# Optimization experiments

Hardware: AMD Instinct MI355X
Metric: run time of the kernel (lower is better)

## Reference

```python
import jax, jax.numpy as jnp
import numpy as np

D = 1024  # feature_size

def setup_inputs() -> dict:
    key = jax.random.key(0)
    ks = jax.random.split(key, 9)
    s = 1.0 / np.sqrt(D)
    inp = {"x": jax.random.normal(ks[0], (4, 2048, D), dtype=jnp.float32)}
    names = ["Wk", "Wq", "Wv", "Wo"]
    for i, n in enumerate(names):
        inp[n] = jax.random.uniform(ks[1 + 2 * i], (D, D), dtype=jnp.float32, minval=-s, maxval=s)
        inp["b" + n[1]] = jax.random.uniform(ks[2 + 2 * i], (D,), dtype=jnp.float32, minval=-s, maxval=s)
    return inp

def reference(x, Wk, bk, Wq, bq, Wv, bv, Wo, bo):
    # Linear layers: x @ W.T + b (torch nn.Linear convention)
    keys = jnp.einsum('bsd,ed->bse', x, Wk) + bk
    queries = jnp.einsum('bsd,ed->bse', x, Wq) + bq
    values = jnp.einsum('bsd,ed->bse', x, Wv) + bv
    scale = 1.0 / jnp.sqrt(jnp.float32(D))
    scores = jnp.einsum('bqd,bkd->bqk', queries, keys) * scale  # [B,S,S]
    attention = jax.nn.softmax(scores, axis=-1)
    out = jnp.einsum('bqk,bkd->bqd', attention, values)
    out = jnp.einsum('bsd,ed->bse', out, Wo) + bo
    return (out, attention)
```

## Files before the change

kernel.cpp:

```cpp
#include <hip/hip_runtime.h>
#include <hip/hip_bf16.h>


typedef __attribute__((ext_vector_type(8))) _Float16 f16x8;
typedef __attribute__((ext_vector_type(4))) _Float16 f16x4;
typedef __attribute__((ext_vector_type(4))) float f32x4;

static __device__ __forceinline__ void gl_lds16(const void* g, void* s) {
  __builtin_amdgcn_global_load_lds(
      (const __attribute__((address_space(1))) void*)g,
      (__attribute__((address_space(3))) void*)s, 16, 0, 0);
}

__global__ __launch_bounds__(256) void prep(
    const float* __restrict__ x,
    const float* __restrict__ Wq, const float* __restrict__ Wk,
    const float* __restrict__ Wo, const float* __restrict__ Wv,
    const float* __restrict__ bv, const float* __restrict__ bo,
    _Float16* __restrict__ xh, _Float16* __restrict__ Woh,
    _Float16* __restrict__ WvT, _Float16* __restrict__ WqT,
    _Float16* __restrict__ WkT, float* __restrict__ cpb) {
  const int b = blockIdx.x;
  const int tid = threadIdx.x;
  if (b < 8192) {
    const int i = b * 256 + tid;
    float4 v = reinterpret_cast<const float4*>(x)[i];
    f16x4 r = {(_Float16)v.x, (_Float16)v.y, (_Float16)v.z, (_Float16)v.w};
    reinterpret_cast<f16x4*>(xh)[i] = r;
  } else if (b < 9216) {
    const int i = (b - 8192) * 256 + tid;
    float4 v = reinterpret_cast<const float4*>(Wo)[i];
    f16x4 r = {(_Float16)v.x, (_Float16)v.y, (_Float16)v.z, (_Float16)v.w};
    reinterpret_cast<f16x4*>(Woh)[i] = r;
  } else if (b < 9984) {
    const int bb = b - 9216;
    const int which = bb >> 8;
    const float* src = which == 0 ? Wv : which == 1 ? Wq : Wk;
    _Float16* dst = which == 0 ? WvT : which == 1 ? WqT : WkT;
    __shared__ float t[64][65];
    const int tb = bb & 255;
    const int bx = (tb & 15) * 64, by = (tb >> 4) * 64;
    const int tx = tid & 63, ty = tid >> 6;
#pragma unroll
    for (int i = 0; i < 64; i += 4)
      t[ty + i][tx] = src[(long)(by + ty + i) * 1024 + bx + tx];
    __syncthreads();
#pragma unroll
    for (int i = 0; i < 64; i += 4)
      dst[(long)(bx + ty + i) * 1024 + by + tx] = (_Float16)t[tx][ty + i];
  } else {
    const int n = b - 9984;
    float s = 0.f;
    for (int d = tid; d < 1024; d += 256) s += Wo[(long)n * 1024 + d] * bv[d];
#pragma unroll
    for (int o = 32; o >= 1; o >>= 1) s += __shfl_xor(s, o);
    __shared__ float red[4];
    if ((tid & 63) == 0) red[tid >> 6] = s;
    __syncthreads();
    if (tid == 0) cpb[n] = red[0] + red[1] + red[2] + red[3] + bo[n];
  }
}

__global__ __launch_bounds__(256) void wkern(
    const float* __restrict__ bq, const float* __restrict__ bk,
    const _Float16* __restrict__ WkT, const _Float16* __restrict__ WqT,
    float* __restrict__ w1, float* __restrict__ w2, float* __restrict__ c0) {
  const int b = blockIdx.x;
  const int tid = threadIdx.x;
  float s = 0.f;
  if (b < 1024) {
    for (int e = tid; e < 1024; e += 256) s += bq[e] * (float)WkT[(long)b * 1024 + e];
  } else if (b < 2048) {
    const int d = b - 1024;
    for (int e = tid; e < 1024; e += 256) s += bk[e] * (float)WqT[(long)d * 1024 + e];
  } else {
    for (int e = tid; e < 1024; e += 256) s += bq[e] * bk[e];
  }
#pragma unroll
  for (int o = 32; o >= 1; o >>= 1) s += __shfl_xor(s, o);
  __shared__ float red[4];
  if ((tid & 63) == 0) red[tid >> 6] = s;
  __syncthreads();
  if (tid == 0) {
    const float v = red[0] + red[1] + red[2] + red[3];
    if (b < 1024) w1[b] = v;
    else if (b < 2048) w2[b - 1024] = v;
    else c0[0] = v;
  }
}

__global__ __launch_bounds__(256) void rowcol(
    const _Float16* __restrict__ xh, const float* __restrict__ w1,
    const float* __restrict__ w2, const float* __restrict__ c0,
    float* __restrict__ rowb, float* __restrict__ colb) {
  const long i = blockIdx.x;
  const int tid = threadIdx.x;
  f16x4 xv = reinterpret_cast<const f16x4*>(xh + i * 1024)[tid];
  float4 a1 = reinterpret_cast<const float4*>(w1)[tid];
  float4 a2 = reinterpret_cast<const float4*>(w2)[tid];
  float x0 = (float)xv[0], x1 = (float)xv[1], x2 = (float)xv[2], x3 = (float)xv[3];
  float d1 = x0 * a1.x + x1 * a1.y + x2 * a1.z + x3 * a1.w;
  float d2 = x0 * a2.x + x1 * a2.y + x2 * a2.z + x3 * a2.w;
#pragma unroll
  for (int o = 32; o >= 1; o >>= 1) { d1 += __shfl_xor(d1, o); d2 += __shfl_xor(d2, o); }
  __shared__ float r1[4], r2[4];
  if ((tid & 63) == 0) { r1[tid >> 6] = d1; r2[tid >> 6] = d2; }
  __syncthreads();
  if (tid == 0) {
    colb[i] = (r1[0] + r1[1] + r1[2] + r1[3]) * 0.03125f;
    rowb[i] = (r2[0] + r2[1] + r2[2] + r2[3] + c0[0]) * 0.03125f;
  }
}

template <int EPI>
__global__ __launch_bounds__(512, 2) void gemm256p8(
    const _Float16* __restrict__ A, const _Float16* __restrict__ B,
    const float* __restrict__ colb, const float* __restrict__ rowb,
    _Float16* __restrict__ Ch, _Float16* __restrict__ C3,
    int M, int N, int K, long sA, long sB, long sC, float alpha) {
  __shared__ _Float16 lds[2][2][2][8192];

  const unsigned gx = gridDim.x, gy = gridDim.y;
  const unsigned nwg = gx * gy * gridDim.z;
  unsigned flat = (blockIdx.z * gy + blockIdx.y) * gx + blockIdx.x;
  flat = (flat & 7) * (nwg >> 3) + (flat >> 3);
  const long bz = flat / (gx * gy);
  const unsigned rem = flat % (gx * gy);
  const unsigned byi = rem % gy;
  const unsigned bxi = rem / gy;

  const int tid = threadIdx.x;
  const int w = tid >> 6, lane = tid & 63;
  const int wr = w >> 2, wc = w & 3;
  const int lr = lane & 15, q = lane >> 4;
  const long row0 = (long)byi * 256;
  const long col0 = (long)bxi * 256;
  const int nt = K >> 6;

  const _Float16* pA = A + bz * sA;
  const _Float16* pB = B + bz * sB;

  f32x4 acc[8][4] = {};

  const int r0 = tid >> 2, c0i = ((tid & 3) - (r0 >> 1)) & 3;
  const int s1 = tid + 512;
  const int r1 = s1 >> 2, c1 = ((s1 & 3) - (r1 >> 1)) & 3;

  auto stage = [&](int t, int ab, int kk) {
    if (t >= nt) return;
    const int d = t & 1;
    const _Float16* src = ab ? pB : pA;
    const long base = ab ? col0 : row0;
    const long gk = (long)t * 64 + kk * 32;
    gl_lds16(src + (base + r0) * (long)K + gk + c0i * 8, &lds[d][ab][kk][w << 9]);
    gl_lds16(src + (base + r1) * (long)K + gk + c1 * 8,
             &lds[d][ab][kk][4096 + (w << 9)]);
  };
  auto rd = [&](int d, int ab, int kk, int r) -> f16x8 {
    const int slot = (r << 2) + ((q + (r >> 1)) & 3);
    return *(const f16x8*)&lds[d][ab][kk][slot << 3];
  };

#define PH_SYNC()                                         \
  __builtin_amdgcn_s_barrier();                           \
  asm volatile("s_waitcnt lgkmcnt(0)" ::: "memory");      \
  __builtin_amdgcn_sched_barrier(0);                      \
  __builtin_amdgcn_s_setprio(1);
#define PH_END()                                          \
  __builtin_amdgcn_s_setprio(0);                          \
  __builtin_amdgcn_sched_barrier(0);                      \
  __builtin_amdgcn_s_barrier();

  stage(0, 0, 0); stage(0, 1, 0); stage(0, 0, 1); stage(0, 1, 1);
  stage(1, 1, 0); stage(1, 0, 0); stage(1, 1, 1);
  asm volatile("s_waitcnt vmcnt(6)" ::: "memory");
  __builtin_amdgcn_s_barrier();
  __builtin_amdgcn_sched_barrier(0);

  f16x8 a[4], b[4];
  for (int t = 0; t < nt; ++t) {
    const int d = t & 1;
#pragma unroll
    for (int mi = 0; mi < 4; ++mi) a[mi] = rd(d, 0, 0, wr * 128 + mi * 16 + lr);
#pragma unroll
    for (int n = 0; n < 4; ++n) b[n] = rd(d, 1, 0, wc * 64 + n * 16 + lr);
    stage(t + 1, 0, 1);
    PH_SYNC();
#pragma unroll
    for (int mi = 0; mi < 4; ++mi)
#pragma unroll
      for (int n = 0; n < 4; ++n)
        acc[mi][n] = __builtin_amdgcn_mfma_f32_16x16x32_f16(a[mi], b[n], acc[mi][n], 0, 0, 0);
    PH_END();
#pragma unroll
    for (int mi = 0; mi < 4; ++mi) a[mi] = rd(d, 0, 0, wr * 128 + 64 + mi * 16 + lr);
    stage(t + 2, 1, 0);
    PH_SYNC();
#pragma unroll
    for (int mi = 0; mi < 4; ++mi)
#pragma unroll
      for (int n = 0; n < 4; ++n)
        acc[4 + mi][n] = __builtin_amdgcn_mfma_f32_16x16x32_f16(a[mi], b[n], acc[4 + mi][n], 0, 0, 0);
    PH_END();
#pragma unroll
    for (int mi = 0; mi < 4; ++mi) a[mi] = rd(d, 0, 1, wr * 128 + mi * 16 + lr);
#pragma unroll
    for (int n = 0; n < 4; ++n) b[n] = rd(d, 1, 1, wc * 64 + n * 16 + lr);
    stage(t + 2, 0, 0);
    PH_SYNC();
#pragma unroll
    for (int mi = 0; mi < 4; ++mi)
#pragma unroll
      for (int n = 0; n < 4; ++n)
        acc[mi][n] = __builtin_amdgcn_mfma_f32_16x16x32_f16(a[mi], b[n], acc[mi][n], 0, 0, 0);
    PH_END();
#pragma unroll
    for (int mi = 0; mi < 4; ++mi) a[mi] = rd(d, 0, 1, wr * 128 + 64 + mi * 16 + lr);
    stage(t + 2, 1, 1);
    PH_SYNC();
#pragma unroll
    for (int mi = 0; mi < 4; ++mi)
#pragma unroll
      for (int n = 0; n < 4; ++n)
        acc[4 + mi][n] = __builtin_amdgcn_mfma_f32_16x16x32_f16(a[mi], b[n], acc[4 + mi][n], 0, 0, 0);
    __builtin_amdgcn_s_setprio(0);
    __builtin_amdgcn_sched_barrier(0);
    if (t + 2 < nt) asm volatile("s_waitcnt vmcnt(6)" ::: "memory");
    else            asm volatile("s_waitcnt vmcnt(0)" ::: "memory");
    __builtin_amdgcn_s_barrier();
    __builtin_amdgcn_sched_barrier(0);
  }
#undef PH_SYNC
#undef PH_END

  if (EPI == 2) {
#pragma unroll
    for (int mi = 0; mi < 8; ++mi)
#pragma unroll
      for (int n = 0; n < 4; ++n)
#pragma unroll
        for (int r = 0; r < 4; ++r) {
          const long row = row0 + wr * 128 + mi * 16 + q * 4 + r;
          const long col = col0 + wc * 64 + n * 16 + lr;
          float v = acc[mi][n][r] * alpha;
          v += rowb[bz * 2048 + row] + colb[bz * 2048 + col];
          Ch[bz * sC + row * (long)N + col] = (_Float16)v;
        }
  } else {
    if (col0 < 1024) {
#pragma unroll
      for (int mi = 0; mi < 8; ++mi)
#pragma unroll
        for (int n = 0; n < 4; ++n)
#pragma unroll
          for (int r = 0; r < 4; ++r) {
            const long row = row0 + wr * 128 + mi * 16 + q * 4 + r;
            const long col = col0 + wc * 64 + n * 16 + lr;
            Ch[row * 1024 + col] = (_Float16)(acc[mi][n][r] * alpha);
          }
    } else {
      _Float16* wb = ((_Float16*)lds) + w * 4224;
      const long b2 = row0 >> 11;
      const long s2b = (row0 & 2047) + wr * 128;
#pragma unroll
      for (int ch = 0; ch < 2; ++ch) {
#pragma unroll
        for (int nn = 0; nn < 2; ++nn) {
          const int n = ch * 2 + nn;
#pragma unroll
          for (int mi = 0; mi < 8; ++mi)
#pragma unroll
            for (int r = 0; r < 4; ++r) {
              const int cl = nn * 16 + lr;
              const int rl = mi * 16 + q * 4 + r;
              wb[cl * 132 + rl] = (_Float16)(acc[mi][n][r] * alpha);
            }
        }
        asm volatile("s_waitcnt lgkmcnt(0)" ::: "memory");
        __builtin_amdgcn_sched_barrier(0);
        const int cl = lane >> 1, sseg = (lane & 1) * 64;
        _Float16* dst = C3 +
            (b2 * 1024 + (col0 - 1024) + wc * 64 + ch * 32 + cl) * 2048 + s2b + sseg;
        const _Float16* srcp = wb + cl * 132 + sseg;
#pragma unroll
        for (int j = 0; j < 8; ++j)
          *(f16x8*)(dst + j * 8) = *(const f16x8*)(srcp + j * 8);
      }
    }
  }
}

__global__ __launch_bounds__(512, 1) void pv128x256(
    const _Float16* __restrict__ P, const _Float16* __restrict__ V,
    const float* __restrict__ cpb, float* __restrict__ out, int K) {
  __shared__ _Float16 lds[2][2][12288];

  const unsigned gx = gridDim.x, gy = gridDim.y;
  const unsigned nwg = gx * gy;
  unsigned flat = blockIdx.y * gx + blockIdx.x;
  flat = (flat & 7) * (nwg >> 3) + (flat >> 3);
  const unsigned byi = flat % gy;
  const unsigned bxi = flat / gy;

  const int tid = threadIdx.x;
  const int w = tid >> 6, lane = tid & 63;
  const int wr = w >> 2, wc = w & 3;
  const int lr = lane & 15, q = lane >> 4;
  const long row0 = (long)byi * 128;
  const long col0 = (long)bxi * 256;
  const int nt = K >> 6;

  const _Float16* pA = P + row0 * (long)K;
  const _Float16* pB = V + (row0 >> 11) * 2097152L + col0 * (long)K;

  f32x4 acc[4][4] = {};

  const int rA = tid >> 2, cA = ((tid & 3) - (rA >> 1)) & 3;
  const int sB1 = tid + 512;
  const int rB1 = sB1 >> 2, cB1 = ((sB1 & 3) - (rB1 >> 1)) & 3;

  auto stage = [&](int t, int kk) {
    if (t >= nt) return;
    const int d = t & 1;
    const long gk = (long)t * 64 + kk * 32;
    gl_lds16(pA + rA * (long)K + gk + cA * 8, &lds[d][kk][w << 9]);
    gl_lds16(pB + rA * (long)K + gk + cA * 8, &lds[d][kk][4096 + (w << 9)]);
    gl_lds16(pB + rB1 * (long)K + gk + cB1 * 8, &lds[d][kk][8192 + (w << 9)]);
  };
  auto rdA = [&](int d, int kk, int r) -> f16x8 {
    const int slot = (r << 2) + ((q + (r >> 1)) & 3);
    return *(const f16x8*)&lds[d][kk][slot << 3];
  };
  auto rdB = [&](int d, int kk, int r) -> f16x8 {
    const int slot = (r << 2) + ((q + (r >> 1)) & 3);
    return *(const f16x8*)&lds[d][kk][4096 * 8 / 8 + (slot << 3)];
  };

#define PH_SYNC()                                         \
  __builtin_amdgcn_s_barrier();                           \
  asm volatile("s_waitcnt lgkmcnt(0)" ::: "memory");      \
  __builtin_amdgcn_sched_barrier(0);                      \
  __builtin_amdgcn_s_setprio(1);

  stage(0, 0); stage(0, 1); stage(1, 0);
  asm volatile("s_waitcnt vmcnt(6)" ::: "memory");
  __builtin_amdgcn_s_barrier();
  __builtin_amdgcn_sched_barrier(0);

  f16x8 a[4], b[4];
  for (int t = 0; t < nt; ++t) {
    const int d = t & 1;
#pragma unroll
    for (int mi = 0; mi < 4; ++mi) a[mi] = rdA(d, 0, wr * 64 + mi * 16 + lr);
#pragma unroll
    for (int n = 0; n < 4; ++n) b[n] = rdB(d, 0, wc * 64 + n * 16 + lr);
    stage(t + 1, 1);
    PH_SYNC();
#pragma unroll
    for (int mi = 0; mi < 4; ++mi)
#pragma unroll
      for (int n = 0; n < 4; ++n)
        acc[mi][n] = __builtin_amdgcn_mfma_f32_16x16x32_f16(a[mi], b[n], acc[mi][n], 0, 0, 0);
    __builtin_amdgcn_s_setprio(0);
    __builtin_amdgcn_sched_barrier(0);
    if (t + 1 < nt) asm volatile("s_waitcnt vmcnt(6)" ::: "memory");
    else            asm volatile("s_waitcnt vmcnt(0)" ::: "memory");
    __builtin_amdgcn_s_barrier();
    __builtin_amdgcn_sched_barrier(0);
#pragma unroll
    for (int mi = 0; mi < 4; ++mi) a[mi] = rdA(d, 1, wr * 64 + mi * 16 + lr);
#pragma unroll
    for (int n = 0; n < 4; ++n) b[n] = rdB(d, 1, wc * 64 + n * 16 + lr);
    stage(t + 2, 0);
    PH_SYNC();
#pragma unroll
    for (int mi = 0; mi < 4; ++mi)
#pragma unroll
      for (int n = 0; n < 4; ++n)
        acc[mi][n] = __builtin_amdgcn_mfma_f32_16x16x32_f16(a[mi], b[n], acc[mi][n], 0, 0, 0);
    __builtin_amdgcn_s_setprio(0);
    __builtin_amdgcn_sched_barrier(0);
    if (t + 2 < nt)      asm volatile("s_waitcnt vmcnt(6)" ::: "memory");
    else if (t + 1 < nt) asm volatile("s_waitcnt vmcnt(3)" ::: "memory");
    else                 asm volatile("s_waitcnt vmcnt(0)" ::: "memory");
    __builtin_amdgcn_s_barrier();
    __builtin_amdgcn_sched_barrier(0);
  }
#undef PH_SYNC

#pragma unroll
  for (int mi = 0; mi < 4; ++mi)
#pragma unroll
    for (int n = 0; n < 4; ++n)
#pragma unroll
      for (int r = 0; r < 4; ++r) {
        const long row = row0 + wr * 64 + mi * 16 + q * 4 + r;
        const long col = col0 + wc * 64 + n * 16 + lr;
        out[row * 1024 + col] = acc[mi][n][r] + cpb[col];
      }
}

template <int EPI, int BSH>
__global__ __launch_bounds__(256) void gemm128(
    const _Float16* __restrict__ A, const _Float16* __restrict__ B,
    const float* __restrict__ bias, float* __restrict__ Cf,
    _Float16* __restrict__ Ch,
    int M, int N, int K, long sA, long sB, long sC, float alpha, int panelW) {
  __shared__ _Float16 lds[3][2][4096];

  const unsigned gx = gridDim.x, gy = gridDim.y;
  const unsigned nwg = gx * gy * gridDim.z;
  unsigned flat = (blockIdx.z * gy + blockIdx.y) * gx + blockIdx.x;
  flat = (flat & 7) * (nwg >> 3) + (flat >> 3);
  const unsigned pb = gy * panelW;
  const long bz = flat / (gx * gy);
  const unsigned rem = flat % (gx * gy);
  const unsigned pi = rem / pb;
  const unsigned rem2 = rem % pb;
  const unsigned byi = rem2 / panelW;
  const unsigned bxi = pi * panelW + rem2 % panelW;

  const int tid = threadIdx.x;
  const int w = tid >> 6, lane = tid & 63;
  const int wr = w >> 1, wc = w & 1;
  const int lr = lane & 15, q = lane >> 4;
  const long row0 = (long)byi * 128;
  const long col0 = (long)bxi * 128;
  const int nt = K >> 5;

  const _Float16* pA = A + bz * sA;
  const _Float16* pB = BSH ? (B + (row0 >> BSH) * sB) : (B + bz * sB);

  f32x4 acc[4][4] = {};

  const int r0 = tid >> 2, c0i = ((tid & 3) - (r0 >> 1)) & 3;
  const int s1 = tid + 256;
  const int r1 = s1 >> 2, c1 = ((s1 & 3) - (r1 >> 1)) & 3;

  auto stage = [&](int kt) {
    if (kt >= nt) return;
    const int bf = kt % 3;
    const long gk = (long)kt * 32;
#pragma unroll
    for (int ab = 0; ab < 2; ++ab) {
      const _Float16* src = ab ? pB : pA;
      const long base = ab ? col0 : row0;
      gl_lds16(src + (base + r0) * (long)K + gk + c0i * 8, &lds[bf][ab][w << 9]);
      gl_lds16(src + (base + r1) * (long)K + gk + c1 * 8, &lds[bf][ab][2048 + (w << 9)]);
    }
  };
  auto rd = [&](int bf, int ab, int r) -> f16x8 {
    const int slot = (r << 2) + ((q + (r >> 1)) & 3);
    return *(const f16x8*)&lds[bf][ab][slot << 3];
  };

  stage(0); stage(1);
  asm volatile("s_waitcnt vmcnt(4)" ::: "memory");
  __builtin_amdgcn_s_barrier();
  __builtin_amdgcn_sched_barrier(0);

  for (int kt = 0; kt < nt; ++kt) {
    const int bf = kt % 3;
    stage(kt + 2);
    f16x8 a[4], b[4];
#pragma unroll
    for (int m = 0; m < 4; ++m) a[m] = rd(bf, 0, wr * 64 + m * 16 + lr);
#pragma unroll
    for (int n = 0; n < 4; ++n) b[n] = rd(bf, 1, wc * 64 + n * 16 + lr);
#pragma unroll
    for (int m = 0; m < 4; ++m)
#pragma unroll
      for (int n = 0; n < 4; ++n)
        acc[m][n] = __builtin_amdgcn_mfma_f32_16x16x32_f16(a[m], b[n], acc[m][n], 0, 0, 0);
    if (kt < nt - 2) asm volatile("s_waitcnt vmcnt(4)" ::: "memory");
    else             asm volatile("s_waitcnt vmcnt(0)" ::: "memory");
    __builtin_amdgcn_s_barrier();
    __builtin_amdgcn_sched_barrier(0);
  }

#pragma unroll
  for (int m = 0; m < 4; ++m)
#pragma unroll
    for (int n = 0; n < 4; ++n)
#pragma unroll
      for (int r = 0; r < 4; ++r) {
        const long row = row0 + wr * 64 + m * 16 + q * 4 + r;
        const long col = col0 + wc * 64 + n * 16 + lr;
        float v = acc[m][n][r] * alpha;
        if (bias) v += bias[col];
        if (EPI == 0) Cf[bz * sC + row * (long)N + col] = v;
        else          Ch[bz * sC + row * (long)N + col] = (_Float16)v;
      }
}

__global__ __launch_bounds__(256) void softmax16(
    _Float16* __restrict__ Ph, float* __restrict__ attn) {
  const long row = blockIdx.x;
  _Float16* ph = Ph + row * 2048;
  float* ap = attn + row * 2048;
  const int tid = threadIdx.x;
  f16x8 v = reinterpret_cast<const f16x8*>(ph)[tid];
  float x[8];
#pragma unroll
  for (int j = 0; j < 8; ++j) x[j] = (float)v[j];
  float m = x[0];
#pragma unroll
  for (int j = 1; j < 8; ++j) m = fmaxf(m, x[j]);
#pragma unroll
  for (int o = 32; o >= 1; o >>= 1) m = fmaxf(m, __shfl_xor(m, o));
  __shared__ float red[4], red2[4];
  if ((tid & 63) == 0) red[tid >> 6] = m;
  __syncthreads();
  m = fmaxf(fmaxf(red[0], red[1]), fmaxf(red[2], red[3]));
  float s = 0.f;
#pragma unroll
  for (int j = 0; j < 8; ++j) { x[j] = expf(x[j] - m); s += x[j]; }
#pragma unroll
  for (int o = 32; o >= 1; o >>= 1) s += __shfl_xor(s, o);
  if ((tid & 63) == 0) red2[tid >> 6] = s;
  __syncthreads();
  s = red2[0] + red2[1] + red2[2] + red2[3];
  const float inv = 1.0f / s;
#pragma unroll
  for (int j = 0; j < 8; ++j) x[j] *= inv;
  reinterpret_cast<float4*>(ap)[tid * 2] = make_float4(x[0], x[1], x[2], x[3]);
  reinterpret_cast<float4*>(ap)[tid * 2 + 1] = make_float4(x[4], x[5], x[6], x[7]);
  f16x8 pv;
#pragma unroll
  for (int j = 0; j < 8; ++j) pv[j] = (_Float16)x[j];
  reinterpret_cast<f16x8*>(ph)[tid] = pv;
}

extern "C" void kernel_launch(void* const* d_in, const int* in_sizes, int n_in,
                              void* d_out, int out_size, void* d_ws, size_t ws_size,
                              hipStream_t stream) {
  const float* x  = (const float*)d_in[0];
  const float* Wk = (const float*)d_in[1];
  const float* bk = (const float*)d_in[2];
  const float* Wq = (const float*)d_in[3];
  const float* bq = (const float*)d_in[4];
  const float* Wv = (const float*)d_in[5];
  const float* bv = (const float*)d_in[6];
  const float* Wo = (const float*)d_in[7];
  const float* bo = (const float*)d_in[8];

  float* out  = (float*)d_out;
  float* attn = (float*)d_out + 8388608;

  const size_t MB = 1024 * 1024;
  unsigned char* ws = (unsigned char*)d_ws;
  _Float16* xh   = (_Float16*)(ws + 0 * MB);
  _Float16* Wf   = (_Float16*)(ws + 16 * MB);
  _Float16* WkT  = (_Float16*)(ws + 20 * MB);
  _Float16* Woh  = (_Float16*)(ws + 22 * MB);
  _Float16* WqT  = (_Float16*)(ws + 24 * MB);
  _Float16* WvT  = (_Float16*)(ws + 26 * MB);
  float*    rowb = (float*)   (ws + 28 * MB);
  float*    colb = (float*)   (ws + 28 * MB + 32768);
  float*    cpb  = (float*)   (ws + 28 * MB + 65536);
  float*    w1   = (float*)   (ws + 28 * MB + 69632);
  float*    w2   = (float*)   (ws + 28 * MB + 73728);
  float*    c0s  = (float*)   (ws + 28 * MB + 77824);
  _Float16* Y    = (_Float16*)(ws + 29 * MB);
  _Float16* Vt   = (_Float16*)(ws + 45 * MB);
  _Float16* Ph   = (_Float16*)(ws + 61 * MB);

  dim3 blk(256);
  dim3 blk5(512);
  const _Float16* nullh = nullptr;

  hipLaunchKernelGGL(prep, dim3(11008), blk, 0, stream,
                     x, Wq, Wk, Wo, Wv, bv, bo, xh, Woh, WvT, WqT, WkT, cpb);
  hipLaunchKernelGGL(wkern, dim3(2049), blk, 0, stream, bq, bk, WkT, WqT, w1, w2, c0s);
  hipLaunchKernelGGL((gemm128<1, 10>), dim3(8, 16, 1), blk, 0, stream,
                     WkT, WqT, (const float*)nullptr, (float*)nullptr, Wf,
                     2048, 1024, 1024, 0L, 1048576L, 0L, 1.0f, 8);
  hipLaunchKernelGGL(rowcol, dim3(8192), blk, 0, stream, xh, w1, w2, c0s, rowb, colb);
  hipLaunchKernelGGL((gemm256p8<3>), dim3(8, 32, 1), blk5, 0, stream,
                     xh, Wf, (const float*)nullptr, (const float*)nullptr, Y, Vt,
                     8192, 2048, 1024, 0L, 0L, 0L, 1.0f);
  hipLaunchKernelGGL((gemm256p8<2>), dim3(8, 8, 4), blk5, 0, stream,
                     Y, xh, colb, rowb, Ph, (_Float16*)nullh,
                     2048, 2048, 1024, 2097152L, 2097152L, 4194304L, 0.03125f);
  hipLaunchKernelGGL(softmax16, dim3(8192), blk, 0, stream, Ph, attn);
  hipLaunchKernelGGL(pv128x256, dim3(4, 64), blk5, 0, stream,
                     Ph, Vt, cpb, out, 2048);
}
```

Baseline: 196.8 us.

## Triple-buffer PV GEMM LDS and prefetch two k-tiles ahead per iteration

Expands the PV kernel's shared-memory ring from two to three 64-wide K stages and issues both halves of tile t+2 while computing tile t. Each iteration now has a single barrier pair with 32 MFMAs, instead of two half-phases of 16 MFMAs each. The aim is to hide global load latency and cut synchronization overhead. In exchange, LDS use rises to about 144KB, register pressure grows from the extra a2/b2 fragments, and the modulo-3 indexing costs a few extra instructions.

```diff
diff --git a/kernel.cpp b/kernel.cpp
--- a/kernel.cpp
+++ b/kernel.cpp
@@ -293,7 +293,7 @@
 __global__ __launch_bounds__(512, 1) void pv128x256(
     const _Float16* __restrict__ P, const _Float16* __restrict__ V,
     const float* __restrict__ cpb, float* __restrict__ out, int K) {
-  __shared__ _Float16 lds[2][2][12288];
+  __shared__ _Float16 lds[3][2][12288];
 
   const unsigned gx = gridDim.x, gy = gridDim.y;
   const unsigned nwg = gx * gy;
@@ -321,7 +321,7 @@
 
   auto stage = [&](int t, int kk) {
     if (t >= nt) return;
-    const int d = t & 1;
+    const int d = t % 3;
     const long gk = (long)t * 64 + kk * 32;
     gl_lds16(pA + rA * (long)K + gk + cA * 8, &lds[d][kk][w << 9]);
     gl_lds16(pB + rA * (long)K + gk + cA * 8, &lds[d][kk][4096 + (w << 9)]);
@@ -333,60 +333,47 @@
   };
   auto rdB = [&](int d, int kk, int r) -> f16x8 {
     const int slot = (r << 2) + ((q + (r >> 1)) & 3);
-    return *(const f16x8*)&lds[d][kk][4096 * 8 / 8 + (slot << 3)];
-  };
-
-#define PH_SYNC()                                         \
-  __builtin_amdgcn_s_barrier();                           \
-  asm volatile("s_waitcnt lgkmcnt(0)" ::: "memory");      \
-  __builtin_amdgcn_sched_barrier(0);                      \
-  __builtin_amdgcn_s_setprio(1);
-
-  stage(0, 0); stage(0, 1); stage(1, 0);
+    return *(const f16x8*)&lds[d][kk][4096 + (slot << 3)];
+  };
+
+  stage(0, 0); stage(0, 1); stage(1, 0); stage(1, 1);
   asm volatile("s_waitcnt vmcnt(6)" ::: "memory");
   __builtin_amdgcn_s_barrier();
   __builtin_amdgcn_sched_barrier(0);
 
-  f16x8 a[4], b[4];
+  f16x8 a[4], b[4], a2[4], b2[4];
   for (int t = 0; t < nt; ++t) {
-    const int d = t & 1;
+    const int d = t % 3;
 #pragma unroll
     for (int mi = 0; mi < 4; ++mi) a[mi] = rdA(d, 0, wr * 64 + mi * 16 + lr);
 #pragma unroll
     for (int n = 0; n < 4; ++n) b[n] = rdB(d, 0, wc * 64 + n * 16 + lr);
-    stage(t + 1, 1);
-    PH_SYNC();
+#pragma unroll
+    for (int mi = 0; mi < 4; ++mi) a2[mi] = rdA(d, 1, wr * 64 + mi * 16 + lr);
+#pragma unroll
+    for (int n = 0; n < 4; ++n) b2[n] = rdB(d, 1, wc * 64 + n * 16 + lr);
+    stage(t + 2, 0); stage(t + 2, 1);
+    __builtin_amdgcn_s_barrier();
+    asm volatile("s_waitcnt lgkmcnt(0)" ::: "memory");
+    __builtin_amdgcn_sched_barrier(0);
+    __builtin_amdgcn_s_setprio(1);
 #pragma unroll
     for (int mi = 0; mi < 4; ++mi)
 #pragma unroll
       for (int n = 0; n < 4; ++n)
         acc[mi][n] = __builtin_amdgcn_mfma_f32_16x16x32_f16(a[mi], b[n], acc[mi][n], 0, 0, 0);
+#pragma unroll
+    for (int mi = 0; mi < 4; ++mi)
+#pragma unroll
+      for (int n = 0; n < 4; ++n)
+        acc[mi][n] = __builtin_amdgcn_mfma_f32_16x16x32_f16(a2[mi], b2[n], acc[mi][n], 0, 0, 0);
     __builtin_amdgcn_s_setprio(0);
     __builtin_amdgcn_sched_barrier(0);
-    if (t + 1 < nt) asm volatile("s_waitcnt vmcnt(6)" ::: "memory");
+    if (t + 2 < nt) asm volatile("s_waitcnt vmcnt(6)" ::: "memory");
     else            asm volatile("s_waitcnt vmcnt(0)" ::: "memory");
     __builtin_amdgcn_s_barrier();
     __builtin_amdgcn_sched_barrier(0);
-#pragma unroll
-    for (int mi = 0; mi < 4; ++mi) a[mi] = rdA(d, 1, wr * 64 + mi * 16 + lr);
-#pragma unroll
-    for (int n = 0; n < 4; ++n) b[n] = rdB(d, 1, wc * 64 + n * 16 + lr);
-    stage(t + 2, 0);
-    PH_SYNC();
-#pragma unroll
-    for (int mi = 0; mi < 4; ++mi)
-#pragma unroll
-      for (int n = 0; n < 4; ++n)
-        acc[mi][n] = __builtin_amdgcn_mfma_f32_16x16x32_f16(a[mi], b[n], acc[mi][n], 0, 0, 0);
-    __builtin_amdgcn_s_setprio(0);
-    __builtin_amdgcn_sched_barrier(0);
-    if (t + 2 < nt)      asm volatile("s_waitcnt vmcnt(6)" ::: "memory");
-    else if (t + 1 < nt) asm volatile("s_waitcnt vmcnt(3)" ::: "memory");
-    else                 asm volatile("s_waitcnt vmcnt(0)" ::: "memory");
-    __builtin_amdgcn_s_barrier();
-    __builtin_amdgcn_sched_barrier(0);
-  }
-#undef PH_SYNC
+  }
 
 #pragma unroll
   for (int mi = 0; mi < 4; ++mi)
```

Measured after the change: 198.9 us. No clear change (+1.1%).
